# Optimization experiments

Measured on AMD Instinct MI355X. Metric: run time of the kernel, lower is better.

The kernel has to match this reference:

```python
import jax, jax.numpy as jnp
import numpy as np

EMBED_DIM = 512
LQ, LA, T, B = 32, 16, 32, 8192
BN_EPS = 1e-5


def _masked_mean(x, lens):
    # x: [L, B, D] seq-first; lens: [B] int. Mean over the first lens[b] steps.
    L = x.shape[0]
    mask = (jnp.arange(L)[:, None] < lens[None, :]).astype(x.dtype)  # [L, B]
    s = jnp.einsum('lb,lbd->bd', mask, x)
    return s / lens.astype(x.dtype)[:, None]


def setup_inputs() -> dict:
    key = jax.random.key(0)
    ks = jax.random.split(key, 12)
    D = EMBED_DIM
    inp = {
        'question_embedding_v': jax.random.normal(ks[0], (LQ, B, D), jnp.float32),
        'visual_embedding_qu': jax.random.normal(ks[1], (T, B, D), jnp.float32),
        'question_len': jax.random.randint(ks[2], (B,), 1, LQ + 1),
        'answer_embedding_v_expand': jax.random.normal(ks[3], (LA, B, D), jnp.float32),
        'visual_embedding_an_expand': jax.random.normal(ks[4], (T, B, D), jnp.float32),
        'answers_len': jax.random.randint(ks[5], (B,), 1, LA + 1),
    }
    # Classifier params (xavier-normal linears, zero bias; BN gamma=1, beta=0)
    def xavier(k, fan_out, fan_in):
        std = (2.0 / (fan_in + fan_out)) ** 0.5
        return std * jax.random.normal(k, (fan_out, fan_in), jnp.float32)
    inp['W1'] = xavier(ks[6], D, 4 * D)
    inp['b1'] = jnp.zeros((D,), jnp.float32)
    inp['gamma'] = jnp.ones((D,), jnp.float32)
    inp['beta'] = jnp.zeros((D,), jnp.float32)
    inp['W2'] = xavier(ks[7], 1, D)
    inp['b2'] = jnp.zeros((1,), jnp.float32)
    return inp


def reference(question_embedding_v, visual_embedding_qu, question_len,
              answer_embedding_v_expand, visual_embedding_an_expand, answers_len,
              W1, b1, gamma, beta, W2, b2):
    q = _masked_mean(question_embedding_v, question_len)            # [B, D]
    vq = jnp.mean(visual_embedding_qu, axis=0)                      # [B, D]
    a = _masked_mean(answer_embedding_v_expand, answers_len)        # [B, D]
    va = jnp.mean(visual_embedding_an_expand, axis=0)               # [B, D]
    out = jnp.concatenate([q, vq, a, va], axis=1)                   # [B, 4D]
    # Dropout treated as identity (eval / deterministic baseline).
    h = out @ W1.T + b1                                             # [B, D]
    h = jax.nn.gelu(h, approximate=False)                           # torch nn.GELU (exact erf)
    # BatchNorm1d in training mode: biased batch statistics over B.
    mu = jnp.mean(h, axis=0)
    var = jnp.mean(jnp.square(h - mu), axis=0)
    h = (h - mu) * jax.lax.rsqrt(var + BN_EPS) * gamma + beta
    logits = h @ W2.T + b2                                          # [B, 1]
    return logits
```

## Files before the change

kernel.cpp:

```cpp
#include <hip/hip_runtime.h>
#include <hip/hip_bf16.h>
#include <math.h>

typedef unsigned short u16;
typedef unsigned int   u32;
typedef short  short8 __attribute__((ext_vector_type(8)));
typedef float  f32x4  __attribute__((ext_vector_type(4)));

#define EMB 512
#define BB  8192
#define KDIM 2048

__device__ inline u16 f2b(float f) {
    union { float f; u32 u; } v; v.f = f;
    u32 r = v.u + 0x7fffu + ((v.u >> 16) & 1u);
    return (u16)(r >> 16);
}

__device__ inline f32x4 ntload(const float* p) {
    return __builtin_nontemporal_load((const f32x4*)p);
}

__global__ __launch_bounds__(256) void k_w1(const float4* __restrict__ w, u16* __restrict__ o) {
    int i = blockIdx.x * 256 + threadIdx.x;
    float4 v = w[i];
    u32 lo = (u32)f2b(v.x) | ((u32)f2b(v.y) << 16);
    u32 hi = (u32)f2b(v.z) | ((u32)f2b(v.w) << 16);
    *(uint2*)(o + (size_t)i * 4) = make_uint2(lo, hi);
}

__global__ __launch_bounds__(256) void k_meanfull(const float* __restrict__ vqu,
                                                  const float* __restrict__ van,
                                                  u16* __restrict__ pooled)
{
    const int tid = threadIdx.x;
    const int ln  = tid & 63;
    int bid = blockIdx.x;
    const float* src; int sec;
    if (bid < 256) { src = vqu; sec = 1; }
    else           { src = van; sec = 3; bid -= 256; }
    const int g = bid * 4 + (tid >> 6);
    const size_t rowf = (size_t)BB * EMB;

    f32x4 acc[16];
    #pragma unroll
    for (int j = 0; j < 16; ++j) acc[j] = (f32x4){0.f, 0.f, 0.f, 0.f};

    const float* p0 = src + (size_t)g * 4096 + ln * 4;
    for (int l = 0; l < 32; ++l) {
        const float* p = p0 + (size_t)l * rowf;
        f32x4 v[16];
        #pragma unroll
        for (int j = 0; j < 16; ++j) v[j] = ntload(p + j * 256);
        #pragma unroll
        for (int j = 0; j < 16; ++j) acc[j] += v[j];
    }

    const int bA = g * 8;
    const float iv = 1.0f / 32.0f;
    #pragma unroll
    for (int j = 0; j < 16; ++j) {
        f32x4 a = acc[j];
        u16* dst = pooled + (size_t)(bA + (j >> 1)) * KDIM + sec * EMB
                 + (j & 1) * 256 + ln * 4;
        *(uint2*)dst = make_uint2((u32)f2b(a.x*iv) | ((u32)f2b(a.y*iv) << 16),
                                  (u32)f2b(a.z*iv) | ((u32)f2b(a.w*iv) << 16));
    }
}

__global__ __launch_bounds__(256) void k_meanmask(
    const float* __restrict__ qv, const int* __restrict__ qlen,
    const float* __restrict__ av, const int* __restrict__ alen,
    u16* __restrict__ pooled)
{
    const int tid  = threadIdx.x;
    const int w    = tid >> 6;
    const int lane = tid & 63;
    const int bA   = blockIdx.x * 16 + w * 4;
    const size_t rowf = (size_t)BB * EMB;

    {
        const int n0 = __builtin_amdgcn_readfirstlane(qlen[bA]);
        const int n1 = __builtin_amdgcn_readfirstlane(qlen[bA + 1]);
        const int n2 = __builtin_amdgcn_readfirstlane(qlen[bA + 2]);
        const int n3 = __builtin_amdgcn_readfirstlane(qlen[bA + 3]);
        int mx = n0 > n1 ? n0 : n1;
        mx = mx > n2 ? mx : n2; mx = mx > n3 ? mx : n3;
        f32x4 a0 = {0,0,0,0}, b0 = a0, a1 = a0, b1 = a0,
              a2 = a0, b2 = a0, a3 = a0, b3 = a0;
        const float* p = qv + (size_t)bA * EMB + lane * 4;
        for (int l = 0; l < mx; ++l) {
            const float* r = p + (size_t)l * rowf;
            if (l < n0) { f32x4 v = ntload(r),        u = ntload(r + 256);  a0 += v; b0 += u; }
            if (l < n1) { f32x4 v = ntload(r + 512),  u = ntload(r + 768);  a1 += v; b1 += u; }
            if (l < n2) { f32x4 v = ntload(r + 1024), u = ntload(r + 1280); a2 += v; b2 += u; }
            if (l < n3) { f32x4 v = ntload(r + 1536), u = ntload(r + 1792); a3 += v; b3 += u; }
        }
        const float i0 = 1.0f/(float)n0, i1 = 1.0f/(float)n1,
                    i2 = 1.0f/(float)n2, i3 = 1.0f/(float)n3;
        u16* d0 = pooled + (size_t)(bA    ) * KDIM + lane * 4;
        u16* d1 = pooled + (size_t)(bA + 1) * KDIM + lane * 4;
        u16* d2 = pooled + (size_t)(bA + 2) * KDIM + lane * 4;
        u16* d3 = pooled + (size_t)(bA + 3) * KDIM + lane * 4;
        *(uint2*)(d0      ) = make_uint2((u32)f2b(a0.x*i0) | ((u32)f2b(a0.y*i0) << 16),
                                         (u32)f2b(a0.z*i0) | ((u32)f2b(a0.w*i0) << 16));
        *(uint2*)(d0 + 256) = make_uint2((u32)f2b(b0.x*i0) | ((u32)f2b(b0.y*i0) << 16),
                                         (u32)f2b(b0.z*i0) | ((u32)f2b(b0.w*i0) << 16));
        *(uint2*)(d1      ) = make_uint2((u32)f2b(a1.x*i1) | ((u32)f2b(a1.y*i1) << 16),
                                         (u32)f2b(a1.z*i1) | ((u32)f2b(a1.w*i1) << 16));
        *(uint2*)(d1 + 256) = make_uint2((u32)f2b(b1.x*i1) | ((u32)f2b(b1.y*i1) << 16),
                                         (u32)f2b(b1.z*i1) | ((u32)f2b(b1.w*i1) << 16));
        *(uint2*)(d2      ) = make_uint2((u32)f2b(a2.x*i2) | ((u32)f2b(a2.y*i2) << 16),
                                         (u32)f2b(a2.z*i2) | ((u32)f2b(a2.w*i2) << 16));
        *(uint2*)(d2 + 256) = make_uint2((u32)f2b(b2.x*i2) | ((u32)f2b(b2.y*i2) << 16),
                                         (u32)f2b(b2.z*i2) | ((u32)f2b(b2.w*i2) << 16));
        *(uint2*)(d3      ) = make_uint2((u32)f2b(a3.x*i3) | ((u32)f2b(a3.y*i3) << 16),
                                         (u32)f2b(a3.z*i3) | ((u32)f2b(a3.w*i3) << 16));
        *(uint2*)(d3 + 256) = make_uint2((u32)f2b(b3.x*i3) | ((u32)f2b(b3.y*i3) << 16),
                                         (u32)f2b(b3.z*i3) | ((u32)f2b(b3.w*i3) << 16));
    }
    {
        const int n0 = __builtin_amdgcn_readfirstlane(alen[bA]);
        const int n1 = __builtin_amdgcn_readfirstlane(alen[bA + 1]);
        const int n2 = __builtin_amdgcn_readfirstlane(alen[bA + 2]);
        const int n3 = __builtin_amdgcn_readfirstlane(alen[bA + 3]);
        int mx = n0 > n1 ? n0 : n1;
        mx = mx > n2 ? mx : n2; mx = mx > n3 ? mx : n3;
        f32x4 a0 = {0,0,0,0}, b0 = a0, a1 = a0, b1 = a0,
              a2 = a0, b2 = a0, a3 = a0, b3 = a0;
        const float* p = av + (size_t)bA * EMB + lane * 4;
        for (int l = 0; l < mx; ++l) {
            const float* r = p + (size_t)l * rowf;
            if (l < n0) { f32x4 v = ntload(r),        u = ntload(r + 256);  a0 += v; b0 += u; }
            if (l < n1) { f32x4 v = ntload(r + 512),  u = ntload(r + 768);  a1 += v; b1 += u; }
            if (l < n2) { f32x4 v = ntload(r + 1024), u = ntload(r + 1280); a2 += v; b2 += u; }
            if (l < n3) { f32x4 v = ntload(r + 1536), u = ntload(r + 1792); a3 += v; b3 += u; }
        }
        const float i0 = 1.0f/(float)n0, i1 = 1.0f/(float)n1,
                    i2 = 1.0f/(float)n2, i3 = 1.0f/(float)n3;
        u16* d0 = pooled + (size_t)(bA    ) * KDIM + 2 * EMB + lane * 4;
        u16* d1 = pooled + (size_t)(bA + 1) * KDIM + 2 * EMB + lane * 4;
        u16* d2 = pooled + (size_t)(bA + 2) * KDIM + 2 * EMB + lane * 4;
        u16* d3 = pooled + (size_t)(bA + 3) * KDIM + 2 * EMB + lane * 4;
        *(uint2*)(d0      ) = make_uint2((u32)f2b(a0.x*i0) | ((u32)f2b(a0.y*i0) << 16),
                                         (u32)f2b(a0.z*i0) | ((u32)f2b(a0.w*i0) << 16));
        *(uint2*)(d0 + 256) = make_uint2((u32)f2b(b0.x*i0) | ((u32)f2b(b0.y*i0) << 16),
                                         (u32)f2b(b0.z*i0) | ((u32)f2b(b0.w*i0) << 16));
        *(uint2*)(d1      ) = make_uint2((u32)f2b(a1.x*i1) | ((u32)f2b(a1.y*i1) << 16),
                                         (u32)f2b(a1.z*i1) | ((u32)f2b(a1.w*i1) << 16));
        *(uint2*)(d1 + 256) = make_uint2((u32)f2b(b1.x*i1) | ((u32)f2b(b1.y*i1) << 16),
                                         (u32)f2b(b1.z*i1) | ((u32)f2b(b1.w*i1) << 16));
        *(uint2*)(d2      ) = make_uint2((u32)f2b(a2.x*i2) | ((u32)f2b(a2.y*i2) << 16),
                                         (u32)f2b(a2.z*i2) | ((u32)f2b(a2.w*i2) << 16));
        *(uint2*)(d2 + 256) = make_uint2((u32)f2b(b2.x*i2) | ((u32)f2b(b2.y*i2) << 16),
                                         (u32)f2b(b2.z*i2) | ((u32)f2b(b2.w*i2) << 16));
        *(uint2*)(d3      ) = make_uint2((u32)f2b(a3.x*i3) | ((u32)f2b(a3.y*i3) << 16),
                                         (u32)f2b(a3.z*i3) | ((u32)f2b(a3.w*i3) << 16));
        *(uint2*)(d3 + 256) = make_uint2((u32)f2b(b3.x*i3) | ((u32)f2b(b3.y*i3) << 16),
                                         (u32)f2b(b3.z*i3) | ((u32)f2b(b3.w*i3) << 16));
    }
}

#define GBM 128
#define GBN 128
#define GBK 64
__global__ __launch_bounds__(256) void k_gemm(
    const u16* __restrict__ A, const u16* __restrict__ Bw,
    const float* __restrict__ bias, float* __restrict__ H)
{
    __shared__ u16 As[GBM * GBK];
    __shared__ u16 Bs[GBN * GBK];

    const int tid  = threadIdx.x;
    const int lane = tid & 63;
    const int wid  = tid >> 6;
    const int wr   = wid >> 1;
    const int wc   = wid & 1;
    const int brow = blockIdx.y * GBM;
    const int bcol = blockIdx.x * GBN;

    const int lrow = lane & 15;
    const int lko  = (lane >> 4) * 8;
    const int gsub = lko >> 3;

    f32x4 acc[4][4];
    #pragma unroll
    for (int m = 0; m < 4; ++m)
        #pragma unroll
        for (int n = 0; n < 4; ++n)
            acc[m][n] = (f32x4){0.f, 0.f, 0.f, 0.f};

    for (int kt = 0; kt < KDIM / GBK; ++kt) {
        const int k0 = kt * GBK;
        #pragma unroll
        for (int i = 0; i < 4; ++i) {
            int f   = i * 256 + tid;
            int row = f >> 3;
            int gl  = (f & 7) ^ (row & 7);
            const u16* srcA = A  + (size_t)(brow + row) * KDIM + k0 + gl * 8;
            const u16* srcB = Bw + (size_t)(bcol + row) * KDIM + k0 + gl * 8;
            __builtin_amdgcn_global_load_lds(
                (const __attribute__((address_space(1))) void*)srcA,
                (__attribute__((address_space(3))) void*)&As[f * 8], 16, 0, 0);
            __builtin_amdgcn_global_load_lds(
                (const __attribute__((address_space(1))) void*)srcB,
                (__attribute__((address_space(3))) void*)&Bs[f * 8], 16, 0, 0);
        }
        __syncthreads();
        #pragma unroll
        for (int kk = 0; kk < 2; ++kk) {
            const int glog = kk * 4 + gsub;
            short8 bfrag[4];
            #pragma unroll
            for (int n = 0; n < 4; ++n) {
                int row = wc * 64 + n * 16 + lrow;
                bfrag[n] = *(const short8*)&Bs[row * GBK + ((glog ^ (row & 7)) * 8)];
            }
            #pragma unroll
            for (int m = 0; m < 4; ++m) {
                int row = wr * 64 + m * 16 + lrow;
                short8 afrag = *(const short8*)&As[row * GBK + ((glog ^ (row & 7)) * 8)];
                #pragma unroll
                for (int n = 0; n < 4; ++n)
                    acc[m][n] = __builtin_amdgcn_mfma_f32_16x16x32_bf16(
                        afrag, bfrag[n], acc[m][n], 0, 0, 0);
            }
        }
        __syncthreads();
    }

    #pragma unroll
    for (int m = 0; m < 4; ++m) {
        const int row0 = brow + wr * 64 + m * 16 + (lane >> 4) * 4;
        #pragma unroll
        for (int n = 0; n < 4; ++n) {
            const int col = bcol + wc * 64 + n * 16 + (lane & 15);
            const float bv = bias[col];
            #pragma unroll
            for (int r = 0; r < 4; ++r) {
                float x = acc[m][n][r] + bv;
                float g = 0.5f * x * (1.0f + erff(x * 0.70710678118654752f));
                H[(size_t)(row0 + r) * EMB + col] = g;
            }
        }
    }
}

__global__ __launch_bounds__(512) void k_stats(const float* __restrict__ H,
                                               float* __restrict__ psum,
                                               float* __restrict__ psq)
{
    const int f = threadIdx.x;
    const int j = blockIdx.x;
    const float* p = H + (size_t)j * 32 * EMB + f;
    float s = 0.f, ss = 0.f;
    #pragma unroll 4
    for (int r = 0; r < 32; ++r) {
        float v = p[(size_t)r * EMB];
        s += v; ss += v * v;
    }
    psum[j * EMB + f] = s;
    psq [j * EMB + f] = ss;
}

__global__ __launch_bounds__(512) void k_fin(const float* __restrict__ psum,
                                             const float* __restrict__ psq,
                                             const float* __restrict__ gamma,
                                             const float* __restrict__ beta,
                                             const float* __restrict__ W2,
                                             const float* __restrict__ b2,
                                             float* __restrict__ coeff)
{
    const int f = threadIdx.x;
    float s = 0.f, ss = 0.f;
    for (int j = 0; j < 256; ++j) { s += psum[j * EMB + f]; ss += psq[j * EMB + f]; }
    const float invB = 1.0f / 8192.0f;
    float mu  = s * invB;
    float var = ss * invB - mu * mu;
    float rs  = rsqrtf(var + 1e-5f);
    float c   = gamma[f] * rs * W2[f];
    coeff[f]  = c;
    float kterm = beta[f] * W2[f] - mu * c;

    __shared__ float red[512];
    red[f] = kterm;
    __syncthreads();
    for (int s2 = 256; s2 > 0; s2 >>= 1) {
        if (f < s2) red[f] += red[f + s2];
        __syncthreads();
    }
    if (f == 0) coeff[512] = red[0] + b2[0];
}

__global__ __launch_bounds__(64) void k_logits(const float* __restrict__ H,
                                               const float* __restrict__ coeff,
                                               float* __restrict__ out)
{
    const int b = blockIdx.x;
    const int l = threadIdx.x;
    const float4* hp = (const float4*)(H + (size_t)b * EMB);
    const float4* cp = (const float4*)coeff;
    float4 h0 = hp[l],      c0 = cp[l];
    float4 h1 = hp[l + 64], c1 = cp[l + 64];
    float p = h0.x * c0.x + h0.y * c0.y + h0.z * c0.z + h0.w * c0.w
            + h1.x * c1.x + h1.y * c1.y + h1.z * c1.z + h1.w * c1.w;
    #pragma unroll
    for (int off = 32; off > 0; off >>= 1) p += __shfl_down(p, off);
    if (l == 0) out[b] = p + coeff[512];
}

extern "C" void kernel_launch(void* const* d_in, const int* in_sizes, int n_in,
                              void* d_out, int out_size, void* d_ws, size_t ws_size,
                              hipStream_t stream) {
    (void)in_sizes; (void)n_in; (void)out_size; (void)ws_size;
    const float* qv    = (const float*)d_in[0];
    const float* vqu   = (const float*)d_in[1];
    const int*   qlen  = (const int*)d_in[2];
    const float* av    = (const float*)d_in[3];
    const float* van   = (const float*)d_in[4];
    const int*   alen  = (const int*)d_in[5];
    const float* W1    = (const float*)d_in[6];
    const float* b1    = (const float*)d_in[7];
    const float* gamma = (const float*)d_in[8];
    const float* beta  = (const float*)d_in[9];
    const float* W2    = (const float*)d_in[10];
    const float* b2    = (const float*)d_in[11];
    float* out = (float*)d_out;

    char* ws = (char*)d_ws;
    u16*   pooled = (u16*)(ws);
    u16*   w1b    = (u16*)(ws + 33554432);
    float* H      = (float*)(ws + 35651584);
    float* psum   = (float*)(ws + 52428800);
    float* psq    = (float*)(ws + 52953088);
    float* coeff  = (float*)(ws + 53477376);

    k_w1      <<<dim3(1024),   dim3(256), 0, stream>>>((const float4*)W1, w1b);
    k_meanfull<<<dim3(512),    dim3(256), 0, stream>>>(vqu, van, pooled);
    k_meanmask<<<dim3(512),    dim3(256), 0, stream>>>(qv, qlen, av, alen, pooled);
    k_gemm    <<<dim3(4, 64),  dim3(256), 0, stream>>>(pooled, w1b, b1, H);
    k_stats   <<<dim3(256),    dim3(512), 0, stream>>>(H, psum, psq);
    k_fin     <<<dim3(1),      dim3(512), 0, stream>>>(psum, psq, gamma, beta, W2, b2, coeff);
    k_logits  <<<dim3(8192),   dim3(64),  0, stream>>>(H, coeff, out);
}
```

Measured before the change: 345.9 us.

## Remap pooling kernels to one thread per float4 with two batch halves

Both pooling kernels now give each thread one float4 column of one batch row, plus the matching row 4096 batches later, instead of a wave walking many rows with large per-thread accumulator arrays. The grid grows from 512 to 2048 blocks, and the accumulator state shrinks from 16 vectors to 2. The aim is more memory-level parallelism and occupancy for this bandwidth-bound reduction, which streams about 1 GB of fp32 input. In the masked kernel, a wave now covers only two sequence lengths, one per half, so it does less wasted looping when lengths differ. The trade-off is fewer independent loads in flight per thread.

```diff
diff --git a/kernel.cpp b/kernel.cpp
--- a/kernel.cpp
+++ b/kernel.cpp
@@ -10,6 +10,8 @@
 #define EMB 512
 #define BB  8192
 #define KDIM 2048
+#define SLICEF 4194304
+#define HALFF  2097152
 
 __device__ inline u16 f2b(float f) {
     union { float f; u32 u; } v; v.f = f;
@@ -19,6 +21,11 @@
 
 __device__ inline f32x4 ntload(const float* p) {
     return __builtin_nontemporal_load((const f32x4*)p);
+}
+
+__device__ inline void store_bf4(u16* dst, f32x4 a, float s) {
+    *(uint2*)dst = make_uint2((u32)f2b(a.x*s) | ((u32)f2b(a.y*s) << 16),
+                              (u32)f2b(a.z*s) | ((u32)f2b(a.w*s) << 16));
 }
 
 __global__ __launch_bounds__(256) void k_w1(const float4* __restrict__ w, u16* __restrict__ o) {
@@ -33,38 +40,36 @@
                                                   const float* __restrict__ van,
                                                   u16* __restrict__ pooled)
 {
-    const int tid = threadIdx.x;
-    const int ln  = tid & 63;
-    int bid = blockIdx.x;
-    const float* src; int sec;
-    if (bid < 256) { src = vqu; sec = 1; }
-    else           { src = van; sec = 3; bid -= 256; }
-    const int g = bid * 4 + (tid >> 6);
-    const size_t rowf = (size_t)BB * EMB;
-
-    f32x4 acc[16];
-    #pragma unroll
-    for (int j = 0; j < 16; ++j) acc[j] = (f32x4){0.f, 0.f, 0.f, 0.f};
-
-    const float* p0 = src + (size_t)g * 4096 + ln * 4;
-    for (int l = 0; l < 32; ++l) {
-        const float* p = p0 + (size_t)l * rowf;
-        f32x4 v[16];
-        #pragma unroll
-        for (int j = 0; j < 16; ++j) v[j] = ntload(p + j * 256);
-        #pragma unroll
-        for (int j = 0; j < 16; ++j) acc[j] += v[j];
-    }
-
-    const int bA = g * 8;
-    const float iv = 1.0f / 32.0f;
-    #pragma unroll
-    for (int j = 0; j < 16; ++j) {
-        f32x4 a = acc[j];
-        u16* dst = pooled + (size_t)(bA + (j >> 1)) * KDIM + sec * EMB
-                 + (j & 1) * 256 + ln * 4;
-        *(uint2*)dst = make_uint2((u32)f2b(a.x*iv) | ((u32)f2b(a.y*iv) << 16),
-                                  (u32)f2b(a.z*iv) | ((u32)f2b(a.w*iv) << 16));
+    const size_t t  = (size_t)blockIdx.x * 256 + threadIdx.x;
+    const int   b0  = (int)(t >> 7);
+    const int   d0  = ((int)t & 127) * 4;
+    const float iv  = 1.0f / 32.0f;
+
+    {
+        const float* p = vqu + t * 4;
+        f32x4 a0 = {0.f,0.f,0.f,0.f}, a1 = a0;
+        #pragma unroll 4
+        for (int l = 0; l < 32; ++l) {
+            const float* r = p + (size_t)l * SLICEF;
+            f32x4 v0 = ntload(r);
+            f32x4 v1 = ntload(r + HALFF);
+            a0 += v0; a1 += v1;
+        }
+        store_bf4(pooled + (size_t)b0 * KDIM + EMB + d0,            a0, iv);
+        store_bf4(pooled + (size_t)(b0 + 4096) * KDIM + EMB + d0,   a1, iv);
+    }
+    {
+        const float* p = van + t * 4;
+        f32x4 a0 = {0.f,0.f,0.f,0.f}, a1 = a0;
+        #pragma unroll 4
+        for (int l = 0; l < 32; ++l) {
+            const float* r = p + (size_t)l * SLICEF;
+            f32x4 v0 = ntload(r);
+            f32x4 v1 = ntload(r + HALFF);
+            a0 += v0; a1 += v1;
+        }
+        store_bf4(pooled + (size_t)b0 * KDIM + 3 * EMB + d0,          a0, iv);
+        store_bf4(pooled + (size_t)(b0 + 4096) * KDIM + 3 * EMB + d0, a1, iv);
     }
 }
 
@@ -73,91 +78,39 @@
     const float* __restrict__ av, const int* __restrict__ alen,
     u16* __restrict__ pooled)
 {
-    const int tid  = threadIdx.x;
-    const int w    = tid >> 6;
-    const int lane = tid & 63;
-    const int bA   = blockIdx.x * 16 + w * 4;
-    const size_t rowf = (size_t)BB * EMB;
-
-    {
-        const int n0 = __builtin_amdgcn_readfirstlane(qlen[bA]);
-        const int n1 = __builtin_amdgcn_readfirstlane(qlen[bA + 1]);
-        const int n2 = __builtin_amdgcn_readfirstlane(qlen[bA + 2]);
-        const int n3 = __builtin_amdgcn_readfirstlane(qlen[bA + 3]);
-        int mx = n0 > n1 ? n0 : n1;
-        mx = mx > n2 ? mx : n2; mx = mx > n3 ? mx : n3;
-        f32x4 a0 = {0,0,0,0}, b0 = a0, a1 = a0, b1 = a0,
-              a2 = a0, b2 = a0, a3 = a0, b3 = a0;
-        const float* p = qv + (size_t)bA * EMB + lane * 4;
+    const size_t t  = (size_t)blockIdx.x * 256 + threadIdx.x;
+    const int   b0  = (int)(t >> 7);
+    const int   d0  = ((int)t & 127) * 4;
+
+    {
+        const int nA = __builtin_amdgcn_readfirstlane(qlen[b0]);
+        const int nB = __builtin_amdgcn_readfirstlane(qlen[b0 + 4096]);
+        const int mx = nA > nB ? nA : nB;
+        const float* p = qv + t * 4;
+        f32x4 a0 = {0.f,0.f,0.f,0.f}, a1 = a0;
+        #pragma unroll 2
         for (int l = 0; l < mx; ++l) {
-            const float* r = p + (size_t)l * rowf;
-            if (l < n0) { f32x4 v = ntload(r),        u = ntload(r + 256);  a0 += v; b0 += u; }
-            if (l < n1) { f32x4 v = ntload(r + 512),  u = ntload(r + 768);  a1 += v; b1 += u; }
-            if (l < n2) { f32x4 v = ntload(r + 1024), u = ntload(r + 1280); a2 += v; b2 += u; }
-            if (l < n3) { f32x4 v = ntload(r + 1536), u = ntload(r + 1792); a3 += v; b3 += u; }
-        }
-        const float i0 = 1.0f/(float)n0, i1 = 1.0f/(float)n1,
-                    i2 = 1.0f/(float)n2, i3 = 1.0f/(float)n3;
-        u16* d0 = pooled + (size_t)(bA    ) * KDIM + lane * 4;
-        u16* d1 = pooled + (size_t)(bA + 1) * KDIM + lane * 4;
-        u16* d2 = pooled + (size_t)(bA + 2) * KDIM + lane * 4;
-        u16* d3 = pooled + (size_t)(bA + 3) * KDIM + lane * 4;
-        *(uint2*)(d0      ) = make_uint2((u32)f2b(a0.x*i0) | ((u32)f2b(a0.y*i0) << 16),
-                                         (u32)f2b(a0.z*i0) | ((u32)f2b(a0.w*i0) << 16));
-        *(uint2*)(d0 + 256) = make_uint2((u32)f2b(b0.x*i0) | ((u32)f2b(b0.y*i0) << 16),
-                                         (u32)f2b(b0.z*i0) | ((u32)f2b(b0.w*i0) << 16));
-        *(uint2*)(d1      ) = make_uint2((u32)f2b(a1.x*i1) | ((u32)f2b(a1.y*i1) << 16),
-                                         (u32)f2b(a1.z*i1) | ((u32)f2b(a1.w*i1) << 16));
-        *(uint2*)(d1 + 256) = make_uint2((u32)f2b(b1.x*i1) | ((u32)f2b(b1.y*i1) << 16),
-                                         (u32)f2b(b1.z*i1) | ((u32)f2b(b1.w*i1) << 16));
-        *(uint2*)(d2      ) = make_uint2((u32)f2b(a2.x*i2) | ((u32)f2b(a2.y*i2) << 16),
-                                         (u32)f2b(a2.z*i2) | ((u32)f2b(a2.w*i2) << 16));
-        *(uint2*)(d2 + 256) = make_uint2((u32)f2b(b2.x*i2) | ((u32)f2b(b2.y*i2) << 16),
-                                         (u32)f2b(b2.z*i2) | ((u32)f2b(b2.w*i2) << 16));
-        *(uint2*)(d3      ) = make_uint2((u32)f2b(a3.x*i3) | ((u32)f2b(a3.y*i3) << 16),
-                                         (u32)f2b(a3.z*i3) | ((u32)f2b(a3.w*i3) << 16));
-        *(uint2*)(d3 + 256) = make_uint2((u32)f2b(b3.x*i3) | ((u32)f2b(b3.y*i3) << 16),
-                                         (u32)f2b(b3.z*i3) | ((u32)f2b(b3.w*i3) << 16));
-    }
-    {
-        const int n0 = __builtin_amdgcn_readfirstlane(alen[bA]);
-        const int n1 = __builtin_amdgcn_readfirstlane(alen[bA + 1]);
-        const int n2 = __builtin_amdgcn_readfirstlane(alen[bA + 2]);
-        const int n3 = __builtin_amdgcn_readfirstlane(alen[bA + 3]);
-        int mx = n0 > n1 ? n0 : n1;
-        mx = mx > n2 ? mx : n2; mx = mx > n3 ? mx : n3;
-        f32x4 a0 = {0,0,0,0}, b0 = a0, a1 = a0, b1 = a0,
-              a2 = a0, b2 = a0, a3 = a0, b3 = a0;
-        const float* p = av + (size_t)bA * EMB + lane * 4;
+            const float* r = p + (size_t)l * SLICEF;
+            if (l < nA) a0 += ntload(r);
+            if (l < nB) a1 += ntload(r + HALFF);
+        }
+        store_bf4(pooled + (size_t)b0 * KDIM + d0,          a0, 1.0f / (float)nA);
+        store_bf4(pooled + (size_t)(b0 + 4096) * KDIM + d0, a1, 1.0f / (float)nB);
+    }
+    {
+        const int nA = __builtin_amdgcn_readfirstlane(alen[b0]);
+        const int nB = __builtin_amdgcn_readfirstlane(alen[b0 + 4096]);
+        const int mx = nA > nB ? nA : nB;
+        const float* p = av + t * 4;
+        f32x4 a0 = {0.f,0.f,0.f,0.f}, a1 = a0;
+        #pragma unroll 2
         for (int l = 0; l < mx; ++l) {
-            const float* r = p + (size_t)l * rowf;
-            if (l < n0) { f32x4 v = ntload(r),        u = ntload(r + 256);  a0 += v; b0 += u; }
-            if (l < n1) { f32x4 v = ntload(r + 512),  u = ntload(r + 768);  a1 += v; b1 += u; }
-            if (l < n2) { f32x4 v = ntload(r + 1024), u = ntload(r + 1280); a2 += v; b2 += u; }
-            if (l < n3) { f32x4 v = ntload(r + 1536), u = ntload(r + 1792); a3 += v; b3 += u; }
-        }
-        const float i0 = 1.0f/(float)n0, i1 = 1.0f/(float)n1,
-                    i2 = 1.0f/(float)n2, i3 = 1.0f/(float)n3;
-        u16* d0 = pooled + (size_t)(bA    ) * KDIM + 2 * EMB + lane * 4;
-        u16* d1 = pooled + (size_t)(bA + 1) * KDIM + 2 * EMB + lane * 4;
-        u16* d2 = pooled + (size_t)(bA + 2) * KDIM + 2 * EMB + lane * 4;
-        u16* d3 = pooled + (size_t)(bA + 3) * KDIM + 2 * EMB + lane * 4;
-        *(uint2*)(d0      ) = make_uint2((u32)f2b(a0.x*i0) | ((u32)f2b(a0.y*i0) << 16),
-                                         (u32)f2b(a0.z*i0) | ((u32)f2b(a0.w*i0) << 16));
-        *(uint2*)(d0 + 256) = make_uint2((u32)f2b(b0.x*i0) | ((u32)f2b(b0.y*i0) << 16),
-                                         (u32)f2b(b0.z*i0) | ((u32)f2b(b0.w*i0) << 16));
-        *(uint2*)(d1      ) = make_uint2((u32)f2b(a1.x*i1) | ((u32)f2b(a1.y*i1) << 16),
-                                         (u32)f2b(a1.z*i1) | ((u32)f2b(a1.w*i1) << 16));
-        *(uint2*)(d1 + 256) = make_uint2((u32)f2b(b1.x*i1) | ((u32)f2b(b1.y*i1) << 16),
-                                         (u32)f2b(b1.z*i1) | ((u32)f2b(b1.w*i1) << 16));
-        *(uint2*)(d2      ) = make_uint2((u32)f2b(a2.x*i2) | ((u32)f2b(a2.y*i2) << 16),
-                                         (u32)f2b(a2.z*i2) | ((u32)f2b(a2.w*i2) << 16));
-        *(uint2*)(d2 + 256) = make_uint2((u32)f2b(b2.x*i2) | ((u32)f2b(b2.y*i2) << 16),
-                                         (u32)f2b(b2.z*i2) | ((u32)f2b(b2.w*i2) << 16));
-        *(uint2*)(d3      ) = make_uint2((u32)f2b(a3.x*i3) | ((u32)f2b(a3.y*i3) << 16),
-                                         (u32)f2b(a3.z*i3) | ((u32)f2b(a3.w*i3) << 16));
-        *(uint2*)(d3 + 256) = make_uint2((u32)f2b(b3.x*i3) | ((u32)f2b(b3.y*i3) << 16),
-                                         (u32)f2b(b3.z*i3) | ((u32)f2b(b3.w*i3) << 16));
+            const float* r = p + (size_t)l * SLICEF;
+            if (l < nA) a0 += ntload(r);
+            if (l < nB) a1 += ntload(r + HALFF);
+        }
+        store_bf4(pooled + (size_t)b0 * KDIM + 2 * EMB + d0,          a0, 1.0f / (float)nA);
+        store_bf4(pooled + (size_t)(b0 + 4096) * KDIM + 2 * EMB + d0, a1, 1.0f / (float)nB);
     }
 }
 
@@ -336,8 +289,8 @@
     float* coeff  = (float*)(ws + 53477376);
 
     k_w1      <<<dim3(1024),   dim3(256), 0, stream>>>((const float4*)W1, w1b);
-    k_meanfull<<<dim3(512),    dim3(256), 0, stream>>>(vqu, van, pooled);
-    k_meanmask<<<dim3(512),    dim3(256), 0, stream>>>(qv, qlen, av, alen, pooled);
+    k_meanfull<<<dim3(2048),   dim3(256), 0, stream>>>(vqu, van, pooled);
+    k_meanmask<<<dim3(2048),   dim3(256), 0, stream>>>(qv, qlen, av, alen, pooled);
     k_gemm    <<<dim3(4, 64),  dim3(256), 0, stream>>>(pooled, w1b, b1, H);
     k_stats   <<<dim3(256),    dim3(512), 0, stream>>>(H, psum, psq);
     k_fin     <<<dim3(1),      dim3(512), 0, stream>>>(psum, psq, gamma, beta, W2, b2, coeff);
```

Measured after the change: 377.9 us, median of 2. 9.3% more time.
